# Optimization experiments

Hardware: AMD Instinct MI355X
Metric: run time of the kernel (lower is better)

Reference implementation:

```python
import jax, jax.numpy as jnp
import numpy as np

D_MODEL = 1024
D_STATE = 16
D_CONV = 4
EXPAND = 2
D_INNER = D_MODEL * EXPAND
DT_RANK = max(D_MODEL // 16, 1)  # 64
B, L = 2, 2048


def setup_inputs() -> dict:
    key = jax.random.key(0)
    ks = jax.random.split(key, 10)
    s = lambda fan_in: 1.0 / np.sqrt(fan_in)
    x = jax.random.normal(ks[0], (B, L, D_MODEL), dtype=jnp.float32)
    ln_w = jnp.ones((D_MODEL,), jnp.float32)
    ln_b = jnp.zeros((D_MODEL,), jnp.float32)
    in_proj_w = jax.random.normal(ks[1], (D_MODEL, 2 * D_INNER), jnp.float32) * s(D_MODEL)
    conv_w = jax.random.normal(ks[2], (D_INNER, D_CONV), jnp.float32) * s(D_CONV)
    conv_b = jnp.zeros((D_INNER,), jnp.float32)
    x_proj_w = jax.random.normal(ks[3], (D_INNER, DT_RANK + 2 * D_STATE), jnp.float32) * s(D_INNER)
    dt_proj_w = jax.random.normal(ks[4], (DT_RANK, D_INNER), jnp.float32) * s(DT_RANK)
    dt_proj_b = jax.random.normal(ks[5], (D_INNER,), jnp.float32) * 0.1
    # A_log init: log(arange(1, d_state+1)) broadcast over d_inner
    A_log = jnp.broadcast_to(jnp.log(jnp.arange(1, D_STATE + 1, dtype=jnp.float32))[None, :], (D_INNER, D_STATE)).copy()
    D_param = jnp.ones((D_INNER,), jnp.float32)
    out_proj_w = jax.random.normal(ks[6], (D_INNER, D_MODEL), jnp.float32) * s(D_INNER)
    res_scale = jnp.ones((1,), jnp.float32)
    return dict(x=x, ln_w=ln_w, ln_b=ln_b, in_proj_w=in_proj_w, conv_w=conv_w,
                conv_b=conv_b, x_proj_w=x_proj_w, dt_proj_w=dt_proj_w,
                dt_proj_b=dt_proj_b, A_log=A_log, D_param=D_param,
                out_proj_w=out_proj_w, res_scale=res_scale)


def _layernorm(x, w, b, eps=1e-5):
    mu = jnp.mean(x, axis=-1, keepdims=True)
    var = jnp.mean(jnp.square(x - mu), axis=-1, keepdims=True)
    return (x - mu) * jax.lax.rsqrt(var + eps) * w + b


def _causal_depthwise_conv1d(x_cl, conv_w, conv_b):
    # x_cl: [B, C, L]; conv_w: [C, K] depthwise; causal left-pad K-1
    out = jax.lax.conv_general_dilated(
        x_cl, conv_w[:, None, :],  # kernel [C,1,K]
        window_strides=(1,), padding=[(D_CONV - 1, 0)],
        dimension_numbers=('NCH', 'OIH', 'NCH'),
        feature_group_count=D_INNER)
    return out + conv_b[None, :, None]


def reference(x, ln_w, ln_b, in_proj_w, conv_w, conv_b, x_proj_w, dt_proj_w,
              dt_proj_b, A_log, D_param, out_proj_w, res_scale):
    residual = x
    xn = _layernorm(x, ln_w, ln_b)                       # [B,L,D]
    xz = xn @ in_proj_w                                  # [B,L,2*Di]
    x_main, z = jnp.split(xz, 2, axis=-1)                # each [B,L,Di]
    x_conv = _causal_depthwise_conv1d(jnp.swapaxes(x_main, 1, 2), conv_w, conv_b)
    new_conv_state = jnp.swapaxes(x_main, 1, 2)[:, :, -(D_CONV - 1):]
    x_main = jax.nn.silu(jnp.swapaxes(x_conv, 1, 2))     # [B,L,Di]

    A = -jnp.exp(A_log)                                  # [Di,N]
    x_dbl = x_main @ x_proj_w                            # [B,L,dt_rank+2N]
    dt, B_ssm, C_ssm = jnp.split(x_dbl, [DT_RANK, DT_RANK + D_STATE], axis=-1)
    dt = jax.nn.softplus(dt @ dt_proj_w + dt_proj_b)     # [B,L,Di]
    dA = jnp.exp(A[None, None] * dt[..., None])          # [B,L,Di,N]
    dBx = dt[..., None] * B_ssm[:, :, None, :] * x_main[..., None]  # [B,L,Di,N]

    def scan_fn(h, inp):
        dA_t, dBx_t, C_t = inp                           # [B,Di,N],[B,Di,N],[B,N]
        h = dA_t * h + dBx_t
        y_t = jnp.einsum('bdn,bn->bd', h, C_t)
        return h, y_t

    h0 = jnp.zeros((x.shape[0], D_INNER, D_STATE), x.dtype)
    new_ssm_state, ys = jax.lax.scan(
        scan_fn, h0,
        (jnp.swapaxes(dA, 0, 1), jnp.swapaxes(dBx, 0, 1), jnp.swapaxes(C_ssm, 0, 1)))
    y = jnp.swapaxes(ys, 0, 1)                           # [B,L,Di]
    y = y + x_main * D_param[None, None, :]
    y = y * jax.nn.silu(z)
    out = res_scale * (y @ out_proj_w) + residual        # [B,L,D]
    return out, new_ssm_state, new_conv_state
```

## Files before the change

kernel.cpp:

```cpp
#include <hip/hip_runtime.h>
#include <math.h>

#define D_MODEL 1024
#define D_STATE 16
#define D_CONVK 4
#define D_INNER 2048
#define DT_RANK 64
#define BB 2
#define LL 2048
#define NROWS (BB*LL)
#define NC 128
#define CH (LL/NC)
#define XZLD 4096
#define LOG2E 1.44269504088896340736f
#define LN2   0.69314718055994530942f

typedef __attribute__((ext_vector_type(8))) short bf16x8;
typedef __attribute__((ext_vector_type(8))) unsigned short u16x8;
typedef __attribute__((ext_vector_type(4))) float f32x4;

typedef __attribute__((address_space(3))) unsigned char lds_ucp;
typedef const __attribute__((address_space(1))) unsigned char glb_ucp;
#define GLD16(gp, lp) __builtin_amdgcn_global_load_lds((glb_ucp*)(gp), (lds_ucp*)(lp), 16, 0, 0)

__device__ inline unsigned short f2bf(float f) {
    union { float f; unsigned u; } c; c.f = f;
    unsigned r = c.u + 0x7fff + ((c.u >> 16) & 1);
    return (unsigned short)(r >> 16);
}
__device__ inline float bf2f(unsigned short s) {
    union { unsigned u; float f; } c; c.u = ((unsigned)s) << 16;
    return c.f;
}
__device__ inline float fexp2(float x) { return __builtin_amdgcn_exp2f(x); }
__device__ inline float frcp(float x)  { return __builtin_amdgcn_rcpf(x); }
__device__ inline float fsilu(float x) { return x * frcp(1.0f + fexp2(-x * LOG2E)); }

__global__ __launch_bounds__(256)
void prologue_kernel(const float* __restrict__ x, const float* __restrict__ lw,
                     const float* __restrict__ lb, unsigned short* __restrict__ xnb,
                     const float* __restrict__ Win, const float* __restrict__ Wout,
                     const float* __restrict__ Wx, const float* __restrict__ Wdt,
                     unsigned short* __restrict__ wtin, unsigned short* __restrict__ wtout,
                     unsigned short* __restrict__ Wxt, unsigned short* __restrict__ Wdtt) {
    if (blockIdx.x < NROWS) {
        int row = blockIdx.x;
        const float* xr = x + (size_t)row * D_MODEL;
        float4 v = ((const float4*)xr)[threadIdx.x];
        float s  = v.x + v.y + v.z + v.w;
        float ss = v.x*v.x + v.y*v.y + v.z*v.z + v.w*v.w;
        for (int off = 32; off > 0; off >>= 1) {
            s  += __shfl_down(s, off);
            ss += __shfl_down(ss, off);
        }
        __shared__ float red[8];
        int lane = threadIdx.x & 63, wv = threadIdx.x >> 6;
        if (lane == 0) { red[wv] = s; red[wv + 4] = ss; }
        __syncthreads();
        if (threadIdx.x == 0) {
            float ts  = red[0] + red[1] + red[2] + red[3];
            float tss = red[4] + red[5] + red[6] + red[7];
            float mu  = ts / D_MODEL;
            float var = tss / D_MODEL - mu * mu;
            red[0] = mu; red[1] = rsqrtf(var + 1e-5f);
        }
        __syncthreads();
        float mu = red[0], rs = red[1];
        float4 w4 = ((const float4*)lw)[threadIdx.x];
        float4 b4 = ((const float4*)lb)[threadIdx.x];
        ushort4 o;
        o.x = f2bf((v.x - mu) * rs * w4.x + b4.x);
        o.y = f2bf((v.y - mu) * rs * w4.y + b4.y);
        o.z = f2bf((v.z - mu) * rs * w4.z + b4.z);
        o.w = f2bf((v.w - mu) * rs * w4.w + b4.w);
        ((ushort4*)(xnb + (size_t)row * D_MODEL))[threadIdx.x] = o;
        return;
    }
    int tb = blockIdx.x - NROWS;
    int bx = tb % 228, by = tb / 228;
    __shared__ float t[32][33];
    const float* W; unsigned short* Wt; int K, Nsrc, xb;
    if (bx < 128)      { W = Win;  Wt = wtin;  K = 1024; Nsrc = 4096; xb = bx; }
    else if (bx < 160) { W = Wout; Wt = wtout; K = 2048; Nsrc = 1024; xb = bx - 128; }
    else if (bx < 164) { W = Wx;   Wt = Wxt;   K = 2048; Nsrc = 96;   xb = bx - 160; }
    else               { W = Wdt;  Wt = Wdtt;  K = 64;   Nsrc = 2048; xb = bx - 164; }
    int k0 = by * 32, n0 = xb * 32;
    if (k0 >= K) return;
    int tx = threadIdx.x & 31, ty = threadIdx.x >> 5;
#pragma unroll
    for (int i = 0; i < 32; i += 8)
        t[ty + i][tx] = (n0 + tx < Nsrc)
            ? W[(size_t)(k0 + ty + i) * Nsrc + n0 + tx] : 0.0f;
    __syncthreads();
#pragma unroll
    for (int i = 0; i < 32; i += 8)
        Wt[(size_t)(n0 + ty + i) * K + k0 + tx] = f2bf(t[tx][ty + i]);
}

__global__ __launch_bounds__(512, 2)
void mfma_gemm_pipe(const unsigned short* __restrict__ A,
                    const unsigned short* __restrict__ Wt,
                    int ldc, int K, unsigned short* __restrict__ out2) {
    __shared__ short As[4][256 * 32];
    __shared__ short Bs[4][256 * 32];
    int tid = threadIdx.x;
    int lane = tid & 63, w = tid >> 6;
    int wm = w & 1, wn = w >> 1;
    int bid = blockIdx.y * gridDim.x + blockIdx.x;
    int cpx = (gridDim.x * gridDim.y) >> 3;
    int swz = (bid & 7) * cpx + (bid >> 3);
    int bx = swz % gridDim.x, by = swz / gridDim.x;
    int row0 = by * 256, col0 = bx * 256;
    const unsigned short* gA0 = A  + (size_t)row0 * K;
    const unsigned short* gB0 = Wt + (size_t)col0 * K;
    int rowin = lane >> 2;
    int scol  = ((lane & 3) ^ ((lane >> 3) & 3)) << 3;
    int quad = lane >> 4, r16 = lane & 15;
    int swr  = (r16 >> 1) & 3;
    int cslot = ((quad ^ swr) << 3);
    f32x4 acc[8][4] = {};
    int nt = K >> 5;

#define STAGE_A(tt) do { int _b = (tt) & 3; int _k0 = (tt) << 5;               \
    _Pragma("unroll")                                                          \
    for (int _l = 0; _l < 2; ++_l) {                                           \
        int _c = _l * 8 + w;                                                   \
        GLD16(gA0 + (size_t)(_c * 16 + rowin) * K + _k0 + scol,                \
              (char*)&As[_b][0] + _c * 1024);                                  \
    } } while (0)
#define STAGE_B(tt) do { int _b = (tt) & 3; int _k0 = (tt) << 5;               \
    _Pragma("unroll")                                                          \
    for (int _l = 0; _l < 2; ++_l) {                                           \
        int _c = _l * 8 + w;                                                   \
        GLD16(gB0 + (size_t)(_c * 16 + rowin) * K + _k0 + scol,                \
              (char*)&Bs[_b][0] + _c * 1024);                                  \
    } } while (0)

    STAGE_A(0); STAGE_B(0); STAGE_A(1); STAGE_B(1);
    asm volatile("s_waitcnt vmcnt(4)" ::: "memory");
    __builtin_amdgcn_s_barrier();

#pragma unroll 4
    for (int t = 0; t < nt; ++t) {
        const short* Ab = &As[t & 3][0];
        const short* Bb = &Bs[t & 3][0];
        bf16x8 bfr[4], af[4];
#pragma unroll
        for (int i = 0; i < 4; ++i)
            bfr[i] = *(const bf16x8*)&Bb[(wn * 64 + i * 16 + r16) * 32 + cslot];
#pragma unroll
        for (int i = 0; i < 4; ++i)
            af[i] = *(const bf16x8*)&Ab[(wm * 128 + i * 16 + r16) * 32 + cslot];
        if (t + 2 < nt) STAGE_A(t + 2);
        __builtin_amdgcn_s_barrier();
        __builtin_amdgcn_s_setprio(1);
#pragma unroll
        for (int mi = 0; mi < 4; ++mi)
#pragma unroll
            for (int ni = 0; ni < 4; ++ni)
                acc[mi][ni] = __builtin_amdgcn_mfma_f32_16x16x32_bf16(
                    af[mi], bfr[ni], acc[mi][ni], 0, 0, 0);
        __builtin_amdgcn_s_setprio(0);
        __builtin_amdgcn_s_barrier();
#pragma unroll
        for (int i = 0; i < 4; ++i)
            af[i] = *(const bf16x8*)&Ab[(wm * 128 + (4 + i) * 16 + r16) * 32 + cslot];
        if (t + 2 < nt) STAGE_B(t + 2);
        __builtin_amdgcn_s_barrier();
        __builtin_amdgcn_s_setprio(1);
#pragma unroll
        for (int mi = 0; mi < 4; ++mi)
#pragma unroll
            for (int ni = 0; ni < 4; ++ni)
                acc[4 + mi][ni] = __builtin_amdgcn_mfma_f32_16x16x32_bf16(
                    af[mi], bfr[ni], acc[4 + mi][ni], 0, 0, 0);
        __builtin_amdgcn_s_setprio(0);
        if (t < nt - 2)       asm volatile("s_waitcnt vmcnt(4)" ::: "memory");
        else if (t == nt - 2) asm volatile("s_waitcnt vmcnt(0)" ::: "memory");
        __builtin_amdgcn_s_barrier();
    }
#undef STAGE_A
#undef STAGE_B
    int odd = lane & 1;
#pragma unroll
    for (int mi = 0; mi < 8; ++mi)
#pragma unroll
        for (int ni = 0; ni < 4; ++ni) {
            int colE = col0 + wn * 64 + ni * 16 + r16;
#pragma unroll
            for (int rp = 0; rp < 2; ++rp) {
                int rowE = row0 + wm * 128 + mi * 16 + quad * 4 + rp * 2;
                int row  = rowE + odd;
                int colp = colE - odd;
                unsigned hh = (unsigned)f2bf(acc[mi][ni][rp*2]) |
                              ((unsigned)f2bf(acc[mi][ni][rp*2+1]) << 16);
                unsigned ph = __shfl_xor((int)hh, 1);
                unsigned u_even = (hh & 0xffffu) | (ph << 16);
                unsigned u_odd  = (ph >> 16) | (hh & 0xffff0000u);
                unsigned u = odd ? u_odd : u_even;
                *(unsigned*)&out2[(size_t)row * ldc + colp] = u;
            }
        }
}

__global__ __launch_bounds__(256)
void mfma_gemm(const unsigned short* __restrict__ A,
               const unsigned short* __restrict__ Wt,
               float* __restrict__ C, int ldc, int K, int kchunk,
               size_t zstride, int mode,
               const float* __restrict__ aux,
               int Ncols, unsigned short* __restrict__ out2) {
    __shared__ short As[128 * 64];
    __shared__ short Bs[128 * 64];
    int tid = threadIdx.x;
    int lane = tid & 63, w = tid >> 6;
    int wm = w & 1, wn = w >> 1;
    int row0 = blockIdx.y * 128, col0 = blockIdx.x * 128;
    int kb = blockIdx.z * kchunk, ke = kb + kchunk;
    C += (size_t)blockIdx.z * zstride;
    f32x4 acc[4][4] = {};
    const unsigned short* gA0 = A  + (size_t)row0 * K;
    const unsigned short* gB0 = Wt + (size_t)col0 * K;
    int r_in = lane >> 3;
    int e16  = (lane & 7) * 8;
    int quad = lane >> 4, r16 = lane & 15;
    for (int k0 = kb; k0 < ke; k0 += 64) {
        __syncthreads();
#pragma unroll
        for (int t = 0; t < 4; ++t) {
            int p = w * 4 + t;
            int row = p * 8 + r_in;
            GLD16(gA0 + (size_t)row * K + k0 + e16, (char*)As + p * 1024);
            GLD16(gB0 + (size_t)row * K + k0 + e16, (char*)Bs + p * 1024);
        }
        __syncthreads();
#pragma unroll
        for (int ks = 0; ks < 2; ++ks) {
            bf16x8 af[4], bfr[4];
#pragma unroll
            for (int i = 0; i < 4; ++i) {
                af[i]  = *(const bf16x8*)&As[(wm * 64 + i * 16 + r16) * 64 + ks * 32 + quad * 8];
                bfr[i] = *(const bf16x8*)&Bs[(wn * 64 + i * 16 + r16) * 64 + ks * 32 + quad * 8];
            }
#pragma unroll
            for (int mi = 0; mi < 4; ++mi)
#pragma unroll
                for (int ni = 0; ni < 4; ++ni)
                    acc[mi][ni] = __builtin_amdgcn_mfma_f32_16x16x32_bf16(
                        af[mi], bfr[ni], acc[mi][ni], 0, 0, 0);
        }
    }
    int odd = lane & 1;
#pragma unroll
    for (int mi = 0; mi < 4; ++mi)
#pragma unroll
        for (int ni = 0; ni < 4; ++ni) {
            int colE = col0 + wn * 64 + ni * 16 + r16;
            float v[4];
#pragma unroll
            for (int r = 0; r < 4; ++r) v[r] = acc[mi][ni][r];
            if (mode == 4) {
                float bv = aux[colE];
#pragma unroll
                for (int r = 0; r < 4; ++r) {
                    float tv = v[r] + bv;
                    v[r] = (tv > 20.0f) ? tv
                         : LN2 * __builtin_amdgcn_logf(1.0f + fexp2(tv * LOG2E));
                }
            }
#pragma unroll
            for (int rp = 0; rp < 2; ++rp) {
                int rowE = row0 + wm * 64 + mi * 16 + quad * 4 + rp * 2;
                int row  = rowE + odd;
                int colp = colE - odd;
                if (mode >= 3) {
                    unsigned hh = (unsigned)f2bf(v[rp*2]) | ((unsigned)f2bf(v[rp*2+1]) << 16);
                    unsigned ph = __shfl_xor((int)hh, 1);
                    unsigned u_even = (hh & 0xffffu) | (ph << 16);
                    unsigned u_odd  = (ph >> 16) | (hh & 0xffff0000u);
                    unsigned u = odd ? u_odd : u_even;
                    *(unsigned*)&out2[(size_t)row * ldc + colp] = u;
                } else {
                    float a0 = v[rp*2], a1 = v[rp*2+1];
                    float b0 = __shfl_xor(a0, 1), b1 = __shfl_xor(a1, 1);
                    float2 f2;
                    f2.x = odd ? b1 : a0;
                    f2.y = odd ? a1 : b0;
                    if (colp < Ncols)
                        *(float2*)&C[(size_t)row * ldc + colp] = f2;
                }
            }
        }
}

__global__ __launch_bounds__(256)
void xdbl_reduce(const float* __restrict__ P,
                 unsigned short* __restrict__ xdtr, float* __restrict__ xbc) {
    const int S1 = NROWS * 96;
    int t = blockIdx.x * 256 + threadIdx.x;
    float s = 0.0f;
#pragma unroll
    for (int k = 0; k < 8; ++k) s += P[t + k * S1];
    int row = t / 96, col = t - row * 96;
    if (col < DT_RANK) xdtr[(size_t)row * DT_RANK + col] = f2bf(s);
    else xbc[(size_t)row * 32 + col - DT_RANK] = s;
}

__global__ __launch_bounds__(256)
void out_final(const float* __restrict__ P0, const float* __restrict__ P1,
               const float* __restrict__ x, const float* __restrict__ rscale,
               float* __restrict__ out) {
    int t = blockIdx.x * 256 + threadIdx.x;
    float rs = rscale[0];
    float4 a = ((const float4*)P0)[t];
    float4 b = ((const float4*)P1)[t];
    float4 r = ((const float4*)x)[t];
    float4 o;
    o.x = rs * (a.x + b.x) + r.x;
    o.y = rs * (a.y + b.y) + r.y;
    o.z = rs * (a.z + b.z) + r.z;
    o.w = rs * (a.w + b.w) + r.w;
    ((float4*)out)[t] = o;
}

__global__ __launch_bounds__(256)
void conv_kernel(const unsigned short* __restrict__ xzb, const float* __restrict__ cw,
                 const float* __restrict__ cb, unsigned short* __restrict__ xs,
                 float* __restrict__ conv_state_out) {
    int loct = blockIdx.x & 255;
    int b    = blockIdx.x >> 8;
    int d0   = threadIdx.x * 8;
    float wgt[8][4];
#pragma unroll
    for (int j = 0; j < 8; ++j) {
        float4 w4 = *(const float4*)(cw + (size_t)(d0 + j) * 4);
        wgt[j][0] = w4.x; wgt[j][1] = w4.y; wgt[j][2] = w4.z; wgt[j][3] = w4.w;
    }
    float bias[8];
    *(float4*)&bias[0] = *(const float4*)(cb + d0);
    *(float4*)&bias[4] = *(const float4*)(cb + d0 + 4);
    float xr[11][8];
#pragma unroll
    for (int r = 0; r < 11; ++r) {
        int l = loct * 8 - 3 + r;
        if (l >= 0) {
            u16x8 v = *(const u16x8*)&xzb[((size_t)b * LL + l) * XZLD + d0];
#pragma unroll
            for (int j = 0; j < 8; ++j) xr[r][j] = bf2f(v[j]);
        } else {
#pragma unroll
            for (int j = 0; j < 8; ++j) xr[r][j] = 0.0f;
        }
    }
#pragma unroll
    for (int i = 0; i < 8; ++i) {
        unsigned short o[8];
#pragma unroll
        for (int j = 0; j < 8; ++j) {
            float a = bias[j];
#pragma unroll
            for (int k = 0; k < 4; ++k) a = fmaf(xr[i + k][j], wgt[j][k], a);
            o[j] = f2bf(fsilu(a));
        }
        *(u16x8*)&xs[((size_t)b * LL + loct * 8 + i) * D_INNER + d0] = *(u16x8*)o;
    }
    if (loct == 255) {
#pragma unroll
        for (int i = 8; i < 11; ++i)
#pragma unroll
            for (int j = 0; j < 8; ++j)
                conv_state_out[((size_t)b * D_INNER + d0 + j) * 3 + (i - 8)] = xr[i][j];
    }
}

__global__ __launch_bounds__(256)
void scan_part1(const unsigned short* __restrict__ dt, const float* __restrict__ xbc,
                const unsigned short* __restrict__ xs,
                const float* __restrict__ A_log,
                float* __restrict__ Sbuf, float* __restrict__ Tbuf) {
    __shared__ float Bs[CH][32];
    int d = blockIdx.x * 256 + threadIdx.x;
    int c = blockIdx.y, b = blockIdx.z;
    size_t rowbase = (size_t)b * LL + (size_t)c * CH;
    for (int e = threadIdx.x; e < CH * 32; e += 256) {
        int i = e >> 5, j = e & 31;
        Bs[i][j] = xbc[(rowbase + i) * 32 + j];
    }
    float al2[16];
    {
        const float4* ap = (const float4*)(A_log + (size_t)d * D_STATE);
#pragma unroll
        for (int q = 0; q < 4; ++q) {
            float4 a4 = ap[q];
            al2[q*4+0] = -fexp2(a4.x * LOG2E) * LOG2E;
            al2[q*4+1] = -fexp2(a4.y * LOG2E) * LOG2E;
            al2[q*4+2] = -fexp2(a4.z * LOG2E) * LOG2E;
            al2[q*4+3] = -fexp2(a4.w * LOG2E) * LOG2E;
        }
    }
    __syncthreads();
    float S[16];
#pragma unroll
    for (int n = 0; n < 16; ++n) S[n] = 0.0f;
    float Tsum = 0.0f;
    float dtv = bf2f(dt[rowbase * D_INNER + d]);
    float xv  = bf2f(xs[rowbase * D_INNER + d]);
    for (int i = 0; i < CH; ++i) {
        float dtn = 0.0f, xn2 = 0.0f;
        if (i + 1 < CH) {
            size_t r2 = (rowbase + i + 1) * D_INNER + d;
            dtn = bf2f(dt[r2]); xn2 = bf2f(xs[r2]);
        }
        Tsum += dtv;
        float dtx = dtv * xv;
#pragma unroll
        for (int q = 0; q < 4; ++q) {
            float4 Bv = *(const float4*)&Bs[i][q * 4];
            S[q*4+0] = fmaf(fexp2(al2[q*4+0] * dtv), S[q*4+0], dtx * Bv.x);
            S[q*4+1] = fmaf(fexp2(al2[q*4+1] * dtv), S[q*4+1], dtx * Bv.y);
            S[q*4+2] = fmaf(fexp2(al2[q*4+2] * dtv), S[q*4+2], dtx * Bv.z);
            S[q*4+3] = fmaf(fexp2(al2[q*4+3] * dtv), S[q*4+3], dtx * Bv.w);
        }
        dtv = dtn; xv = xn2;
    }
    size_t o = (((size_t)b * NC + c) * D_INNER + d) * D_STATE;
#pragma unroll
    for (int q = 0; q < 4; ++q) {
        float4 Sv;
        Sv.x = S[q*4+0]; Sv.y = S[q*4+1]; Sv.z = S[q*4+2]; Sv.w = S[q*4+3];
        *(float4*)(Sbuf + o + q * 4) = Sv;
    }
    Tbuf[((size_t)b * NC + c) * D_INNER + d] = Tsum;
}

__global__ __launch_bounds__(256)
void scan_part2(const float* __restrict__ S, const float* __restrict__ Tbuf,
                const float* __restrict__ A_log, float* __restrict__ Hin) {
    int t = blockIdx.x * 256 + threadIdx.x;
    int b = t >> 15;
    int rem = t & 32767;
    int d = rem >> 4;
    float al2 = -fexp2(A_log[rem] * LOG2E) * LOG2E;
    size_t sbase = (size_t)b * NC * (D_INNER * D_STATE) + rem;
    size_t tbase = (size_t)b * NC * D_INNER + d;
    float h = 0.0f;
    for (int c = 0; c < NC; ++c) {
        size_t sq = sbase + (size_t)c * (D_INNER * D_STATE);
        float s = S[sq];
        float T = Tbuf[tbase + (size_t)c * D_INNER];
        Hin[sq] = h;
        h = fmaf(fexp2(al2 * T), h, s);
    }
}

__global__ __launch_bounds__(256)
void scan_part3(const unsigned short* __restrict__ dt, const float* __restrict__ xbc,
                const unsigned short* __restrict__ xs,
                const unsigned short* __restrict__ xzb,
                const float* __restrict__ A_log, const float* __restrict__ Dp,
                const float* __restrict__ Hin,
                unsigned short* __restrict__ y, float* __restrict__ ssm_out) {
    __shared__ float Bs[CH][32];
    int d = blockIdx.x * 256 + threadIdx.x;
    int c = blockIdx.y, b = blockIdx.z;
    size_t rowbase = (size_t)b * LL + (size_t)c * CH;
    for (int e = threadIdx.x; e < CH * 32; e += 256) {
        int i = e >> 5, j = e & 31;
        Bs[i][j] = xbc[(rowbase + i) * 32 + j];
    }
    float al2[16];
    {
        const float4* ap = (const float4*)(A_log + (size_t)d * D_STATE);
#pragma unroll
        for (int q = 0; q < 4; ++q) {
            float4 a4 = ap[q];
            al2[q*4+0] = -fexp2(a4.x * LOG2E) * LOG2E;
            al2[q*4+1] = -fexp2(a4.y * LOG2E) * LOG2E;
            al2[q*4+2] = -fexp2(a4.z * LOG2E) * LOG2E;
            al2[q*4+3] = -fexp2(a4.w * LOG2E) * LOG2E;
        }
    }
    float Dv = Dp[d];
    float h[16];
    {
        const float4* hp = (const float4*)(Hin + (((size_t)b * NC + c) * D_INNER + d) * D_STATE);
#pragma unroll
        for (int q = 0; q < 4; ++q) {
            float4 h4 = hp[q];
            h[q*4+0] = h4.x; h[q*4+1] = h4.y; h[q*4+2] = h4.z; h[q*4+3] = h4.w;
        }
    }
    __syncthreads();
    size_t r0 = rowbase * D_INNER + d;
    float dtv = bf2f(dt[r0]);
    float xv  = bf2f(xs[r0]);
    float zv  = bf2f(xzb[rowbase * XZLD + D_INNER + d]);
    for (int i = 0; i < CH; ++i) {
        float dtn = 0.0f, xn2 = 0.0f, zn2 = 0.0f;
        if (i + 1 < CH) {
            size_t r2 = (rowbase + i + 1) * D_INNER + d;
            dtn = bf2f(dt[r2]); xn2 = bf2f(xs[r2]);
            zn2 = bf2f(xzb[(rowbase + i + 1) * XZLD + D_INNER + d]);
        }
        float dtx = dtv * xv;
        float yv = 0.0f;
#pragma unroll
        for (int q = 0; q < 4; ++q) {
            float4 Bv = *(const float4*)&Bs[i][q * 4];
            float4 Cv = *(const float4*)&Bs[i][16 + q * 4];
            h[q*4+0] = fmaf(fexp2(al2[q*4+0] * dtv), h[q*4+0], dtx * Bv.x);
            h[q*4+1] = fmaf(fexp2(al2[q*4+1] * dtv), h[q*4+1], dtx * Bv.y);
            h[q*4+2] = fmaf(fexp2(al2[q*4+2] * dtv), h[q*4+2], dtx * Bv.z);
            h[q*4+3] = fmaf(fexp2(al2[q*4+3] * dtv), h[q*4+3], dtx * Bv.w);
            yv = fmaf(h[q*4+0], Cv.x, yv);
            yv = fmaf(h[q*4+1], Cv.y, yv);
            yv = fmaf(h[q*4+2], Cv.z, yv);
            yv = fmaf(h[q*4+3], Cv.w, yv);
        }
        yv = (yv + xv * Dv) * fsilu(zv);
        y[(rowbase + i) * D_INNER + d] = f2bf(yv);
        dtv = dtn; xv = xn2; zv = zn2;
    }
    if (c == NC - 1) {
        float* sp = ssm_out + ((size_t)b * D_INNER + d) * D_STATE;
#pragma unroll
        for (int q = 0; q < 4; ++q) {
            float4 h4;
            h4.x = h[q*4+0]; h4.y = h[q*4+1]; h4.z = h[q*4+2]; h4.w = h[q*4+3];
            *(float4*)(sp + q * 4) = h4;
        }
    }
}

extern "C" void kernel_launch(void* const* d_in, const int* in_sizes, int n_in,
                              void* d_out, int out_size, void* d_ws, size_t ws_size,
                              hipStream_t stream) {
    (void)in_sizes; (void)n_in; (void)out_size; (void)ws_size;
    const float* x      = (const float*)d_in[0];
    const float* ln_w   = (const float*)d_in[1];
    const float* ln_b   = (const float*)d_in[2];
    const float* Win    = (const float*)d_in[3];
    const float* convw  = (const float*)d_in[4];
    const float* convb  = (const float*)d_in[5];
    const float* Wx     = (const float*)d_in[6];
    const float* Wdt    = (const float*)d_in[7];
    const float* bdt    = (const float*)d_in[8];
    const float* A_log  = (const float*)d_in[9];
    const float* Dp     = (const float*)d_in[10];
    const float* Wout   = (const float*)d_in[11];
    const float* rscale = (const float*)d_in[12];

    float* out      = (float*)d_out;
    float* ssm_out  = out + (size_t)NROWS * D_MODEL;
    float* conv_out = ssm_out + (size_t)BB * D_INNER * D_STATE;

    float* ws = (float*)d_ws;
    unsigned short* xzb = (unsigned short*)ws;
    unsigned short* xsb = xzb + (size_t)NROWS * XZLD;
    unsigned short* dtbb = xsb + (size_t)NROWS * D_INNER;
    float* xbc  = (float*)(dtbb + (size_t)NROWS * D_INNER);
    unsigned short* xdtr = (unsigned short*)(xbc + (size_t)NROWS * 32);
    unsigned short* xnb  = xdtr + (size_t)NROWS * DT_RANK;
    unsigned short* wtin = xnb + (size_t)NROWS * D_MODEL;
    unsigned short* wtout = wtin + (size_t)(2 * D_INNER) * D_MODEL;
    unsigned short* Wxt  = wtout + (size_t)D_MODEL * D_INNER;
    unsigned short* Wdtt = Wxt + (size_t)128 * D_INNER;
    float* Tbuf = (float*)(Wdtt + (size_t)D_INNER * DT_RANK);
    float* Sbuf = Tbuf + (size_t)BB * NC * D_INNER;
    float* Pxdbl = Sbuf;
    float* Hin   = Sbuf;
    float* P0 = Sbuf;
    float* P1 = Sbuf + (size_t)NROWS * D_MODEL;
    unsigned short* ybuf = xnb;

    prologue_kernel<<<NROWS + 228 * 64, 256, 0, stream>>>(
        x, ln_w, ln_b, xnb, Win, Wout, Wx, Wdt, wtin, wtout, Wxt, Wdtt);

    mfma_gemm_pipe<<<dim3(2 * D_INNER / 256, NROWS / 256), 512, 0, stream>>>(
        xnb, wtin, XZLD, D_MODEL, xzb);

    conv_kernel<<<BB * (LL / 8), 256, 0, stream>>>(
        xzb, convw, convb, xsb, conv_out);

    mfma_gemm<<<dim3(1, NROWS / 128, 8), 256, 0, stream>>>(
        xsb, Wxt, Pxdbl, 96, D_INNER, D_INNER / 8, (size_t)NROWS * 96, 0,
        nullptr, 96, nullptr);
    xdbl_reduce<<<(NROWS * 96) / 256, 256, 0, stream>>>(Pxdbl, xdtr, xbc);

    mfma_gemm<<<dim3(D_INNER / 128, NROWS / 128), 256, 0, stream>>>(
        xdtr, Wdtt, nullptr, D_INNER, DT_RANK, DT_RANK, 0, 4,
        bdt, D_INNER, dtbb);

    scan_part1<<<dim3(D_INNER / 256, NC, BB), 256, 0, stream>>>(
        dtbb, xbc, xsb, A_log, Sbuf, Tbuf);
    scan_part2<<<(BB * D_INNER * D_STATE) / 256, 256, 0, stream>>>(
        Sbuf, Tbuf, A_log, Hin);
    scan_part3<<<dim3(D_INNER / 256, NC, BB), 256, 0, stream>>>(
        dtbb, xbc, xsb, xzb, A_log, Dp, Hin, ybuf, ssm_out);

    mfma_gemm<<<dim3(D_MODEL / 128, NROWS / 128, 2), 256, 0, stream>>>(
        ybuf, wtout, P0, D_MODEL, D_INNER, D_INNER / 2,
        (size_t)NROWS * D_MODEL, 0,
        nullptr, D_MODEL, nullptr);

    out_final<<<(NROWS * D_MODEL) / (256 * 4), 256, 0, stream>>>(
        P0, P1, x, rscale, out);
}
```

Baseline: 300.3 us.

## Fuse out_proj GEMM with residual epilogue and halve scan chunk count

Replaces the split-K out-projection GEMM plus separate out_final reduction kernel with a single 512-thread MFMA kernel that runs the full K=2048 reduction and applies res_scale and the residual add in its epilogue. This removes the fp32 partial buffers and one extra launch and pass over memory. It also drops the scan chunk count from 128 to 64, so chunks are longer. That halves the cross-chunk state work but gives fewer blocks in the scan kernels. The new GEMM has no split-K, so it runs only 256 blocks with a long serial K loop and no double-buffering, which may lower occupancy.

```diff
diff --git a/kernel.cpp b/kernel.cpp
--- a/kernel.cpp
+++ b/kernel.cpp
@@ -9,7 +9,7 @@
 #define BB 2
 #define LL 2048
 #define NROWS (BB*LL)
-#define NC 128
+#define NC 64
 #define CH (LL/NC)
 #define XZLD 4096
 #define LOG2E 1.44269504088896340736f
@@ -293,6 +293,77 @@
         }
 }
 
+__global__ __launch_bounds__(512)
+void mfma_out_fused(const unsigned short* __restrict__ A,
+                    const unsigned short* __restrict__ Wt,
+                    const float* __restrict__ x, const float* __restrict__ rscale,
+                    float* __restrict__ out) {
+    __shared__ short As[128 * 64];
+    __shared__ short Bs[128 * 64];
+    const int K = 2 * D_MODEL;
+    int tid = threadIdx.x;
+    int lane = tid & 63, w = tid >> 6;
+    int wm = w & 3, wn = w >> 2;
+    int row0 = blockIdx.y * 128, col0 = blockIdx.x * 128;
+    f32x4 acc[2][4] = {};
+    const unsigned short* gA0 = A  + (size_t)row0 * K;
+    const unsigned short* gB0 = Wt + (size_t)col0 * K;
+    int r_in = lane >> 3;
+    int e16  = (lane & 7) * 8;
+    int quad = lane >> 4, r16 = lane & 15;
+    for (int k0 = 0; k0 < K; k0 += 64) {
+        __syncthreads();
+#pragma unroll
+        for (int t = 0; t < 2; ++t) {
+            int p = w * 2 + t;
+            int row = p * 8 + r_in;
+            GLD16(gA0 + (size_t)row * K + k0 + e16, (char*)As + p * 1024);
+            GLD16(gB0 + (size_t)row * K + k0 + e16, (char*)Bs + p * 1024);
+        }
+        __syncthreads();
+#pragma unroll
+        for (int ks = 0; ks < 2; ++ks) {
+            bf16x8 af[2], bfr[4];
+#pragma unroll
+            for (int i = 0; i < 2; ++i)
+                af[i]  = *(const bf16x8*)&As[(wm * 32 + i * 16 + r16) * 64 + ks * 32 + quad * 8];
+#pragma unroll
+            for (int i = 0; i < 4; ++i)
+                bfr[i] = *(const bf16x8*)&Bs[(wn * 64 + i * 16 + r16) * 64 + ks * 32 + quad * 8];
+#pragma unroll
+            for (int mi = 0; mi < 2; ++mi)
+#pragma unroll
+                for (int ni = 0; ni < 4; ++ni)
+                    acc[mi][ni] = __builtin_amdgcn_mfma_f32_16x16x32_bf16(
+                        af[mi], bfr[ni], acc[mi][ni], 0, 0, 0);
+        }
+    }
+    float rs = rscale[0];
+    int odd = lane & 1;
+#pragma unroll
+    for (int mi = 0; mi < 2; ++mi)
+#pragma unroll
+        for (int ni = 0; ni < 4; ++ni) {
+            int colE = col0 + wn * 64 + ni * 16 + r16;
+#pragma unroll
+            for (int rp = 0; rp < 2; ++rp) {
+                int rowE = row0 + wm * 32 + mi * 16 + quad * 4 + rp * 2;
+                int row  = rowE + odd;
+                int colp = colE - odd;
+                float a0 = acc[mi][ni][rp*2], a1 = acc[mi][ni][rp*2+1];
+                float b0 = __shfl_xor(a0, 1), b1 = __shfl_xor(a1, 1);
+                float2 f2;
+                f2.x = odd ? b1 : a0;
+                f2.y = odd ? a1 : b0;
+                float2 xr = *(const float2*)&x[(size_t)row * D_MODEL + colp];
+                float2 o2;
+                o2.x = rs * f2.x + xr.x;
+                o2.y = rs * f2.y + xr.y;
+                *(float2*)&out[(size_t)row * D_MODEL + colp] = o2;
+            }
+        }
+}
+
 __global__ __launch_bounds__(256)
 void xdbl_reduce(const float* __restrict__ P,
                  unsigned short* __restrict__ xdtr, float* __restrict__ xbc) {
@@ -304,23 +375,6 @@
     int row = t / 96, col = t - row * 96;
     if (col < DT_RANK) xdtr[(size_t)row * DT_RANK + col] = f2bf(s);
     else xbc[(size_t)row * 32 + col - DT_RANK] = s;
-}
-
-__global__ __launch_bounds__(256)
-void out_final(const float* __restrict__ P0, const float* __restrict__ P1,
-               const float* __restrict__ x, const float* __restrict__ rscale,
-               float* __restrict__ out) {
-    int t = blockIdx.x * 256 + threadIdx.x;
-    float rs = rscale[0];
-    float4 a = ((const float4*)P0)[t];
-    float4 b = ((const float4*)P1)[t];
-    float4 r = ((const float4*)x)[t];
-    float4 o;
-    o.x = rs * (a.x + b.x) + r.x;
-    o.y = rs * (a.y + b.y) + r.y;
-    o.z = rs * (a.z + b.z) + r.z;
-    o.w = rs * (a.w + b.w) + r.w;
-    ((float4*)out)[t] = o;
 }
 
 __global__ __launch_bounds__(256)
@@ -569,8 +623,6 @@
     float* Sbuf = Tbuf + (size_t)BB * NC * D_INNER;
     float* Pxdbl = Sbuf;
     float* Hin   = Sbuf;
-    float* P0 = Sbuf;
-    float* P1 = Sbuf + (size_t)NROWS * D_MODEL;
     unsigned short* ybuf = xnb;
 
     prologue_kernel<<<NROWS + 228 * 64, 256, 0, stream>>>(
@@ -598,11 +650,6 @@
     scan_part3<<<dim3(D_INNER / 256, NC, BB), 256, 0, stream>>>(
         dtbb, xbc, xsb, xzb, A_log, Dp, Hin, ybuf, ssm_out);
 
-    mfma_gemm<<<dim3(D_MODEL / 128, NROWS / 128, 2), 256, 0, stream>>>(
-        ybuf, wtout, P0, D_MODEL, D_INNER, D_INNER / 2,
-        (size_t)NROWS * D_MODEL, 0,
-        nullptr, D_MODEL, nullptr);
-
-    out_final<<<(NROWS * D_MODEL) / (256 * 4), 256, 0, stream>>>(
-        P0, P1, x, rscale, out);
-}
+    mfma_out_fused<<<dim3(D_MODEL / 128, NROWS / 128), 512, 0, stream>>>(
+        ybuf, wtout, x, rscale, out);
+}
```

Result: no change. 303.1 us (+0.9%).
